# Kernel optimization log

Hardware: AMD Instinct MI355X
Metric: run time of the kernel (lower is better)

## Reference

```python
import jax, jax.numpy as jnp
import numpy as np

N = 100000
BN_EPS = 1e-5


def gcn_conv(x, W, b, src, dst, dinv):
    # PyG GCNConv: out = D^-1/2 (A+I) D^-1/2 (X W) + b
    h = x @ W                                   # [N, out]
    norm = dinv[src] * dinv[dst]                # [E'] edge weights
    msg = h[src] * norm[:, None]                # gather + scale  [E', out]
    agg = jax.ops.segment_sum(msg, dst, num_segments=N)
    return agg + b


def batch_norm(h, gamma, beta):
    mu = jnp.mean(h, axis=0)
    var = jnp.mean((h - mu) ** 2, axis=0)       # biased var, as torch BN training
    return gamma * (h - mu) * jax.lax.rsqrt(var + BN_EPS) + beta


def setup_inputs() -> dict:
    key = jax.random.key(0)
    ks = jax.random.split(key, 12)
    E = 1600000
    d_in, d_h, d_out = 128, 128, 40
    x = jax.random.normal(ks[0], (N, d_in), dtype=jnp.float32)
    edge_index = jax.random.randint(ks[1], (2, E), 0, N, dtype=jnp.int64)

    def glorot(k, fan_in, fan_out):
        s = jnp.sqrt(6.0 / (fan_in + fan_out))
        return jax.random.uniform(k, (fan_in, fan_out), jnp.float32, -s, s)

    return {
        "x": x,
        "W1": glorot(ks[2], d_in, d_h), "b1": jnp.zeros((d_h,), jnp.float32),
        "W2": glorot(ks[3], d_h, d_h), "b2": jnp.zeros((d_h,), jnp.float32),
        "W3": glorot(ks[4], d_h, d_out), "b3": jnp.zeros((d_out,), jnp.float32),
        "g1": 1.0 + 0.1 * jax.random.normal(ks[5], (d_h,), jnp.float32),
        "be1": 0.1 * jax.random.normal(ks[6], (d_h,), jnp.float32),
        "g2": 1.0 + 0.1 * jax.random.normal(ks[7], (d_h,), jnp.float32),
        "be2": 0.1 * jax.random.normal(ks[8], (d_h,), jnp.float32),
        "edge_index": edge_index,
    }


def reference(x, W1, b1, W2, b2, W3, b3, g1, be1, g2, be2, edge_index):
    # add self loops once (PyG add_self_loops=True)
    loop = jnp.arange(N, dtype=edge_index.dtype)
    src = jnp.concatenate([edge_index[0], loop])
    dst = jnp.concatenate([edge_index[1], loop])
    deg = jax.ops.segment_sum(jnp.ones_like(src, dtype=x.dtype), dst, num_segments=N)
    dinv = jax.lax.rsqrt(deg)                   # deg >= 1 due to self loops

    h = gcn_conv(x, W1, b1, src, dst, dinv)
    h = jax.nn.relu(batch_norm(h, g1, be1))     # dropout: identity at eval
    h = gcn_conv(h, W2, b2, src, dst, dinv)
    h = jax.nn.relu(batch_norm(h, g2, be2))
    h = gcn_conv(h, W3, b3, src, dst, dinv)
    return jax.nn.log_softmax(h, axis=1)
```

## Files before the change

kernel.cpp:

```cpp
#include <hip/hip_runtime.h>
#include <cstdint>
#include <cstddef>


typedef unsigned int uint32;
typedef __attribute__((ext_vector_type(8))) short bf16x8;
typedef __attribute__((ext_vector_type(4))) float f32x4;

__device__ inline float bl(uint32 u) { uint32 v = u << 16; return __builtin_bit_cast(float, v); }
__device__ inline float bh(uint32 u) { uint32 v = u & 0xffff0000u; return __builtin_bit_cast(float, v); }
__device__ inline uint32 f2b(float f) {
    uint32 u = __builtin_bit_cast(uint32, f);
    return (u + 0x7fffu + ((u >> 16) & 1u)) >> 16;
}
__device__ inline uint32 pack2(float x, float y) { return f2b(x) | (f2b(y) << 16); }

#define MFMA16(a, b, c) __builtin_amdgcn_mfma_f32_16x16x32_bf16(a, b, c, 0, 0, 0)
#define CSR_CH 4096
#define NSTAT 1024


__global__ __launch_bounds__(256) void bucket_hist(const int* __restrict__ dst,
                                                   int* __restrict__ bcntp,
                                                   int E, int NB) {
    __shared__ int lh[1024];
    for (int t = threadIdx.x; t < NB; t += 256) lh[t] = 0;
    __syncthreads();
    int stride = gridDim.x * 256;
    for (int e = blockIdx.x * 256 + threadIdx.x; e < E; e += stride)
        atomicAdd(&lh[dst[e] >> 7], 1);
    __syncthreads();
    for (int t = threadIdx.x; t < NB; t += 256)
        if (lh[t]) atomicAdd(&bcntp[t * 16], lh[t]);
}

__global__ __launch_bounds__(1024) void bucket_scan(const int* __restrict__ bcntp,
                                                    int* __restrict__ boffs,
                                                    int* __restrict__ bcurp, int nb) {
    __shared__ int s[1024];
    int tx = threadIdx.x;
    int v = (tx < nb) ? bcntp[tx * 16] : 0;
    s[tx] = v;
    __syncthreads();
    for (int off = 1; off < 1024; off <<= 1) {
        int t = (tx >= off) ? s[tx - off] : 0;
        __syncthreads();
        s[tx] += t;
        __syncthreads();
    }
    if (tx < nb) {
        int ex = s[tx] - v;
        boffs[tx] = ex;
        bcurp[tx * 16] = ex;
    }
    if (tx == 0) boffs[nb] = s[1023];
}

__global__ __launch_bounds__(256) void bucket_fill2(const int* __restrict__ src,
                                                    const int* __restrict__ dst,
                                                    int* __restrict__ bcurp,
                                                    uint32* __restrict__ bkt,
                                                    int E, int NB) {
    __shared__ int lh[1024];
    __shared__ int lcur[1024];
    int e0 = blockIdx.x * CSR_CH;
    int e1 = e0 + CSR_CH;
    if (e1 > E) e1 = E;
    for (int t = threadIdx.x; t < NB; t += 256) lh[t] = 0;
    __syncthreads();
    for (int e = e0 + threadIdx.x; e < e1; e += 256)
        atomicAdd(&lh[dst[e] >> 7], 1);
    __syncthreads();
    for (int t = threadIdx.x; t < NB; t += 256)
        lcur[t] = lh[t] ? atomicAdd(&bcurp[t * 16], lh[t]) : 0;
    __syncthreads();
    for (int e = e0 + threadIdx.x; e < e1; e += 256) {
        int d = dst[e];
        int b = d >> 7;
        int pos = atomicAdd(&lcur[b], 1);
        bkt[pos] = (uint32)src[e] | ((uint32)(d & 127) << 17);
    }
}

__global__ __launch_bounds__(256) void bucket_csr(const uint32* __restrict__ bkt,
                                                  const int* __restrict__ boffs,
                                                  float* __restrict__ dinv,
                                                  int* __restrict__ offs,
                                                  int* __restrict__ csr, int n) {
    __shared__ int lcnt[128];
    __shared__ int lscan[128];
    __shared__ int lcur[128];
    int b = blockIdx.x;
    int tx = threadIdx.x;
    if (tx < 128) lcnt[tx] = 0;
    __syncthreads();
    int j0 = boffs[b], j1 = boffs[b + 1];
    for (int j = j0 + tx; j < j1; j += 256)
        atomicAdd(&lcnt[bkt[j] >> 17], 1);
    __syncthreads();
    if (tx < 128) lscan[tx] = lcnt[tx];
    __syncthreads();
    for (int off = 1; off < 128; off <<= 1) {
        int v = 0;
        if (tx < 128 && tx >= off) v = lscan[tx - off];
        __syncthreads();
        if (tx < 128) lscan[tx] += v;
        __syncthreads();
    }
    if (tx < 128) {
        int node = b * 128 + tx;
        if (node < n) {
            int o = j0 + lscan[tx] - lcnt[tx];
            offs[node] = o;
            lcur[tx] = o;
            dinv[node] = rsqrtf((float)(lcnt[tx] + 1));
        }
    }
    if (b == gridDim.x - 1 && tx == 0) offs[n] = j1;
    __syncthreads();
    for (int j = j0 + tx; j < j1; j += 256) {
        uint32 e = bkt[j];
        int dloc = e >> 17;
        int pos = atomicAdd(&lcur[dloc], 1);
        csr[pos] = (int)(e & 0x1FFFFu);
    }
}

__global__ __launch_bounds__(256) void wconv(const float* __restrict__ W1,
                                             const float* __restrict__ W2,
                                             const float* __restrict__ W3,
                                             unsigned short* __restrict__ wt1,
                                             unsigned short* __restrict__ wt2,
                                             unsigned short* __restrict__ wt3) {
    int b = blockIdx.x, tx = threadIdx.x;
    if (b < 2) {
        const float* S = b ? W2 : W1;
        unsigned short* D = b ? wt2 : wt1;
        for (int i = tx; i < 128 * 128; i += 256) {
            int k = i >> 7, nn = i & 127;
            D[nn * 128 + k] = (unsigned short)f2b(S[i]);
        }
    } else {
        for (int i = tx; i < 48 * 128; i += 256) {
            int k = i / 48, nn = i - k * 48;
            float v = (nn < 40) ? W3[k * 40 + nn] : 0.f;
            wt3[nn * 128 + k] = (unsigned short)f2b(v);
        }
    }
}


template <bool ABF16, bool BN>
__global__ __launch_bounds__(256) void gemm128m(const void* __restrict__ Av,
                                                const unsigned short* __restrict__ WT,
                                                uint32* __restrict__ C,
                                                const float* __restrict__ dinv, int n,
                                                const float* __restrict__ scale,
                                                const float* __restrict__ shift) {
    __shared__ unsigned short Wls[128 * 128];
    __shared__ unsigned short Als[128 * 128];
    int tx = threadIdx.x;
    int row0 = blockIdx.x * 128;
    {
        const uint4* srcW = (const uint4*)WT;
#pragma unroll
        for (int i = 0; i < 8; i++) {
            int cid = tx + 256 * i;
            int nr = cid >> 4, kb = cid & 15;
            uint4 u = srcW[cid];
            *(uint4*)&Wls[nr * 128 + ((kb ^ (nr & 7)) << 3)] = u;
        }
    }
    int kb = tx & 15;
    if (ABF16) {
        const uint4* src = (const uint4*)Av;
        float4 sA, sB, hA_, hB_;
        if (BN) {
            sA = ((const float4*)scale)[kb * 2];
            sB = ((const float4*)scale)[kb * 2 + 1];
            hA_ = ((const float4*)shift)[kb * 2];
            hB_ = ((const float4*)shift)[kb * 2 + 1];
        }
#pragma unroll
        for (int i = 0; i < 8; i++) {
            int r = (tx >> 4) + 16 * i;
            int gr = row0 + r;
            if (gr >= n) gr = n - 1;
            uint4 u = src[(size_t)gr * 16 + kb];
            if (BN) {
                uint4 o;
                o.x = pack2(fmaxf(0.f, bl(u.x) * sA.x + hA_.x), fmaxf(0.f, bh(u.x) * sA.y + hA_.y));
                o.y = pack2(fmaxf(0.f, bl(u.y) * sA.z + hA_.z), fmaxf(0.f, bh(u.y) * sA.w + hA_.w));
                o.z = pack2(fmaxf(0.f, bl(u.z) * sB.x + hB_.x), fmaxf(0.f, bh(u.z) * sB.y + hB_.y));
                o.w = pack2(fmaxf(0.f, bl(u.w) * sB.z + hB_.z), fmaxf(0.f, bh(u.w) * sB.w + hB_.w));
                u = o;
            }
            *(uint4*)&Als[r * 128 + ((kb ^ (r & 7)) << 3)] = u;
        }
    } else {
        const float4* src = (const float4*)Av;
#pragma unroll
        for (int i = 0; i < 8; i++) {
            int r = (tx >> 4) + 16 * i;
            int gr = row0 + r;
            if (gr >= n) gr = n - 1;
            float4 a = src[(size_t)gr * 32 + kb * 2];
            float4 b = src[(size_t)gr * 32 + kb * 2 + 1];
            uint4 u;
            u.x = pack2(a.x, a.y);
            u.y = pack2(a.z, a.w);
            u.z = pack2(b.x, b.y);
            u.w = pack2(b.z, b.w);
            *(uint4*)&Als[r * 128 + ((kb ^ (r & 7)) << 3)] = u;
        }
    }
    __syncthreads();

    int w = tx >> 6, lane = tx & 63;
    int r0 = w * 32;
    int lrow = lane & 15, lkg = lane >> 4;
    f32x4 acc[2][8];
#pragma unroll
    for (int rt = 0; rt < 2; rt++)
#pragma unroll
        for (int nt = 0; nt < 8; nt++) acc[rt][nt] = (f32x4){0.f, 0.f, 0.f, 0.f};
#pragma unroll
    for (int ks = 0; ks < 4; ks++) {
        int kbl = ks * 4 + lkg;
        int r = r0 + lrow;
        bf16x8 a0 = *(const bf16x8*)&Als[r * 128 + ((kbl ^ (r & 7)) << 3)];
        int r2 = r0 + 16 + lrow;
        bf16x8 a1 = *(const bf16x8*)&Als[r2 * 128 + ((kbl ^ (r2 & 7)) << 3)];
#pragma unroll
        for (int nt = 0; nt < 8; nt++) {
            int nr = nt * 16 + lrow;
            bf16x8 b = *(const bf16x8*)&Wls[nr * 128 + ((kbl ^ (nr & 7)) << 3)];
            acc[0][nt] = MFMA16(a0, b, acc[0][nt]);
            acc[1][nt] = MFMA16(a1, b, acc[1][nt]);
        }
    }
    float* SL = (float*)&Als[w * 4096];
#pragma unroll
    for (int rt = 0; rt < 2; rt++) {
#pragma unroll
        for (int nt = 0; nt < 8; nt++)
#pragma unroll
            for (int j = 0; j < 4; j++)
                SL[(lkg * 4 + j) * 128 + nt * 16 + lrow] = acc[rt][nt][j];
#pragma unroll
        for (int i = 0; i < 8; i++) {
            int rloc = i * 2 + (lane >> 5);
            int gr = row0 + r0 + rt * 16 + rloc;
            int cq = lane & 31;
            if (gr < n) {
                float dv = dinv[gr];
                float4 v = *(float4*)&SL[rloc * 128 + cq * 4];
                uint2 o;
                o.x = pack2(v.x * dv, v.y * dv);
                o.y = pack2(v.z * dv, v.w * dv);
                *(uint2*)&C[(size_t)gr * 64 + cq * 2] = o;
            }
        }
        if (rt == 0) __builtin_amdgcn_s_waitcnt(0);
    }
}

__global__ __launch_bounds__(256) void gemm40m(const uint32* __restrict__ A,
                                               const unsigned short* __restrict__ WT,
                                               unsigned short* __restrict__ C,
                                               const float* __restrict__ dinv, int n,
                                               const float* __restrict__ scale,
                                               const float* __restrict__ shift) {
    __shared__ unsigned short Wls[48 * 128];
    __shared__ unsigned short Als[128 * 128];
    int tx = threadIdx.x;
    int row0 = blockIdx.x * 128;
    {
        const uint4* srcW = (const uint4*)WT;
#pragma unroll
        for (int i = 0; i < 3; i++) {
            int cid = tx + 256 * i;
            int nr = cid >> 4, kb = cid & 15;
            uint4 u = srcW[cid];
            *(uint4*)&Wls[nr * 128 + ((kb ^ (nr & 7)) << 3)] = u;
        }
    }
    int kb = tx & 15;
    {
        const uint4* src = (const uint4*)A;
        float4 sA = ((const float4*)scale)[kb * 2];
        float4 sB = ((const float4*)scale)[kb * 2 + 1];
        float4 hA_ = ((const float4*)shift)[kb * 2];
        float4 hB_ = ((const float4*)shift)[kb * 2 + 1];
#pragma unroll
        for (int i = 0; i < 8; i++) {
            int r = (tx >> 4) + 16 * i;
            int gr = row0 + r;
            if (gr >= n) gr = n - 1;
            uint4 u = src[(size_t)gr * 16 + kb];
            uint4 o;
            o.x = pack2(fmaxf(0.f, bl(u.x) * sA.x + hA_.x), fmaxf(0.f, bh(u.x) * sA.y + hA_.y));
            o.y = pack2(fmaxf(0.f, bl(u.y) * sA.z + hA_.z), fmaxf(0.f, bh(u.y) * sA.w + hA_.w));
            o.z = pack2(fmaxf(0.f, bl(u.z) * sB.x + hB_.x), fmaxf(0.f, bh(u.z) * sB.y + hB_.y));
            o.w = pack2(fmaxf(0.f, bl(u.w) * sB.z + hB_.z), fmaxf(0.f, bh(u.w) * sB.w + hB_.w));
            *(uint4*)&Als[r * 128 + ((kb ^ (r & 7)) << 3)] = o;
        }
    }
    __syncthreads();

    int w = tx >> 6, lane = tx & 63;
    int r0 = w * 32;
    int lrow = lane & 15, lkg = lane >> 4;
    f32x4 acc[2][3];
#pragma unroll
    for (int rt = 0; rt < 2; rt++)
#pragma unroll
        for (int nt = 0; nt < 3; nt++) acc[rt][nt] = (f32x4){0.f, 0.f, 0.f, 0.f};
#pragma unroll
    for (int ks = 0; ks < 4; ks++) {
        int kbl = ks * 4 + lkg;
        int r = r0 + lrow;
        bf16x8 a0 = *(const bf16x8*)&Als[r * 128 + ((kbl ^ (r & 7)) << 3)];
        int r2 = r0 + 16 + lrow;
        bf16x8 a1 = *(const bf16x8*)&Als[r2 * 128 + ((kbl ^ (r2 & 7)) << 3)];
#pragma unroll
        for (int nt = 0; nt < 3; nt++) {
            int nr = nt * 16 + lrow;
            bf16x8 b = *(const bf16x8*)&Wls[nr * 128 + ((kbl ^ (nr & 7)) << 3)];
            acc[0][nt] = MFMA16(a0, b, acc[0][nt]);
            acc[1][nt] = MFMA16(a1, b, acc[1][nt]);
        }
    }
#pragma unroll
    for (int rt = 0; rt < 2; rt++)
#pragma unroll
        for (int j = 0; j < 4; j++) {
            int gr = row0 + r0 + rt * 16 + lkg * 4 + j;
            if (gr < n) {
                float dv = dinv[gr];
#pragma unroll
                for (int nt = 0; nt < 3; nt++) {
                    int col = nt * 16 + lrow;
                    if (col < 40)
                        C[(size_t)gr * 40 + col] = (unsigned short)f2b(acc[rt][nt][j] * dv);
                }
            }
        }
}


__global__ __launch_bounds__(256) void agg128(const uint32* __restrict__ h,
                                              const int* __restrict__ csr,
                                              const int* __restrict__ offs,
                                              const float* __restrict__ dinv,
                                              const float* __restrict__ bias,
                                              uint32* __restrict__ out, int n) {
    int wid = (blockIdx.x * 256 + threadIdx.x) >> 6;
    int lane = threadIdx.x & 63;
    if (wid >= n) return;
    int half = lane >> 5;
    int t = lane & 31;
    const uint2* h2 = (const uint2*)h;
    float a0 = 0.f, a1 = 0.f, a2 = 0.f, a3 = 0.f;
    float c0 = 0.f, c1 = 0.f, c2 = 0.f, c3 = 0.f;
    if (half == 0) {
        uint2 u = h2[(size_t)wid * 32 + t];
        a0 = bl(u.x); a1 = bh(u.x); a2 = bl(u.y); a3 = bh(u.y);
    }
    int e0 = offs[wid], e1 = offs[wid + 1];
    int e = e0;
    while (e < e1) {
        int cnt = e1 - e;
        if (cnt > 64) cnt = 64;
        int sl = (lane < cnt) ? csr[e + lane] : 0;
        int j = 0;
        for (; j + 3 < cnt; j += 4) {
            int sa = __shfl(sl, j + half, 64);
            int sb = __shfl(sl, j + 2 + half, 64);
            uint2 ua = h2[(size_t)sa * 32 + t];
            uint2 ub = h2[(size_t)sb * 32 + t];
            a0 += bl(ua.x); a1 += bh(ua.x); a2 += bl(ua.y); a3 += bh(ua.y);
            c0 += bl(ub.x); c1 += bh(ub.x); c2 += bl(ub.y); c3 += bh(ub.y);
        }
        for (; j < cnt; j++) {
            int s = __shfl(sl, j, 64);
            if (half == (j & 1)) {
                uint2 u = h2[(size_t)s * 32 + t];
                a0 += bl(u.x); a1 += bh(u.x); a2 += bl(u.y); a3 += bh(u.y);
            }
        }
        e += cnt;
    }
    a0 += c0; a1 += c1; a2 += c2; a3 += c3;
    a0 += __shfl_xor(a0, 32, 64);
    a1 += __shfl_xor(a1, 32, 64);
    a2 += __shfl_xor(a2, 32, 64);
    a3 += __shfl_xor(a3, 32, 64);
    if (half == 0) {
        float di = dinv[wid];
        float4 bb = ((const float4*)bias)[t];
        uint2 o;
        o.x = pack2(a0 * di + bb.x, a1 * di + bb.y);
        o.y = pack2(a2 * di + bb.z, a3 * di + bb.w);
        ((uint2*)out)[(size_t)wid * 32 + t] = o;
    }
}

__global__ __launch_bounds__(256) void agg40_lsm(const uint32* __restrict__ h,
                                                 const int* __restrict__ csr,
                                                 const int* __restrict__ offs,
                                                 const float* __restrict__ dinv,
                                                 const float* __restrict__ bias,
                                                 float* __restrict__ out, int n) {
    int wid = (blockIdx.x * 256 + threadIdx.x) >> 6;
    int lane = threadIdx.x & 63;
    if (wid >= n) return;
    int grp = lane / 10;
    int t = lane - grp * 10;
    bool work = grp < 6;
    const uint2* h2 = (const uint2*)h;
    float a0 = 0.f, a1 = 0.f, a2 = 0.f, a3 = 0.f;
    if (grp == 0) {
        uint2 u = h2[(size_t)wid * 10 + t];
        a0 = bl(u.x); a1 = bh(u.x); a2 = bl(u.y); a3 = bh(u.y);
    }
    int e0 = offs[wid], e1 = offs[wid + 1];
    int e = e0;
    while (e < e1) {
        int cnt = e1 - e;
        if (cnt > 64) cnt = 64;
        int sl = (lane < cnt) ? csr[e + lane] : 0;
        int nIt = (cnt + 11) / 12;
        for (int it = 0; it < nIt; it++) {
            int j0 = it * 12 + grp;
            int j1 = j0 + 6;
            int s0 = __shfl(sl, (j0 < cnt) ? j0 : 0, 64);
            int s1 = __shfl(sl, (j1 < cnt) ? j1 : 0, 64);
            if (work && j0 < cnt) {
                uint2 u = h2[(size_t)s0 * 10 + t];
                a0 += bl(u.x); a1 += bh(u.x); a2 += bl(u.y); a3 += bh(u.y);
            }
            if (work && j1 < cnt) {
                uint2 u = h2[(size_t)s1 * 10 + t];
                a0 += bl(u.x); a1 += bh(u.x); a2 += bl(u.y); a3 += bh(u.y);
            }
        }
        e += cnt;
    }
    a0 += __shfl(a0, (lane + 30) & 63, 64);
    a1 += __shfl(a1, (lane + 30) & 63, 64);
    a2 += __shfl(a2, (lane + 30) & 63, 64);
    a3 += __shfl(a3, (lane + 30) & 63, 64);
    {
        float t0 = __shfl(a0, (lane + 10) & 63, 64), u0 = __shfl(a0, (lane + 20) & 63, 64);
        float t1 = __shfl(a1, (lane + 10) & 63, 64), u1 = __shfl(a1, (lane + 20) & 63, 64);
        float t2 = __shfl(a2, (lane + 10) & 63, 64), u2 = __shfl(a2, (lane + 20) & 63, 64);
        float t3 = __shfl(a3, (lane + 10) & 63, 64), u3 = __shfl(a3, (lane + 20) & 63, 64);
        a0 += t0 + u0; a1 += t1 + u1; a2 += t2 + u2; a3 += t3 + u3;
    }
    bool act = lane < 10;
    float di = dinv[wid];
    float v0 = -1e30f, v1 = -1e30f, v2 = -1e30f, v3 = -1e30f;
    if (act) {
        float4 bb = ((const float4*)bias)[t];
        v0 = a0 * di + bb.x;
        v1 = a1 * di + bb.y;
        v2 = a2 * di + bb.z;
        v3 = a3 * di + bb.w;
    }
    float m = fmaxf(fmaxf(v0, v1), fmaxf(v2, v3));
    for (int off = 8; off; off >>= 1) m = fmaxf(m, __shfl_xor(m, off, 64));
    float ss = act ? (expf(v0 - m) + expf(v1 - m) + expf(v2 - m) + expf(v3 - m)) : 0.f;
    for (int off = 8; off; off >>= 1) ss += __shfl_xor(ss, off, 64);
    float lg = logf(ss);
    if (act) {
        float4 o = {v0 - m - lg, v1 - m - lg, v2 - m - lg, v3 - m - lg};
        *(float4*)&out[(size_t)wid * 40 + t * 4] = o;
    }
}


__global__ __launch_bounds__(256) void stats_k(const uint32* __restrict__ h,
                                               float* __restrict__ psum,
                                               float* __restrict__ psq, int n) {
    int kb = threadIdx.x & 15;
    int rg = threadIdx.x >> 4;
    float s[8], q[8];
#pragma unroll
    for (int j = 0; j < 8; j++) { s[j] = 0.f; q[j] = 0.f; }
    const uint4* h4 = (const uint4*)h;
    for (int r = blockIdx.x * 16 + rg; r < n; r += gridDim.x * 16) {
        uint4 u = h4[(size_t)r * 16 + kb];
        float f[8] = {bl(u.x), bh(u.x), bl(u.y), bh(u.y),
                      bl(u.z), bh(u.z), bl(u.w), bh(u.w)};
#pragma unroll
        for (int j = 0; j < 8; j++) { s[j] += f[j]; q[j] += f[j] * f[j]; }
    }
    __shared__ float LS[16][16][8];
    __shared__ float LQ[16][16][8];
#pragma unroll
    for (int j = 0; j < 8; j++) { LS[rg][kb][j] = s[j]; LQ[rg][kb][j] = q[j]; }
    __syncthreads();
    if (threadIdx.x < 128) {
        int cq = threadIdx.x >> 3, j = threadIdx.x & 7;
        float S = 0.f, Q = 0.f;
#pragma unroll
        for (int g = 0; g < 16; g++) { S += LS[g][cq][j]; Q += LQ[g][cq][j]; }
        psum[blockIdx.x * 128 + cq * 8 + j] = S;
        psq[blockIdx.x * 128 + cq * 8 + j] = Q;
    }
}

__global__ __launch_bounds__(1024) void finalize_stats(const float* __restrict__ psum,
                                                       const float* __restrict__ psq,
                                                       const float* __restrict__ g,
                                                       const float* __restrict__ be,
                                                       float* __restrict__ scale,
                                                       float* __restrict__ shift,
                                                       int nb, float invN) {
    int c = threadIdx.x & 127;
    int seg = threadIdx.x >> 7;
    int per = nb >> 3;
    float s = 0.f, q = 0.f;
    for (int b = seg * per; b < (seg + 1) * per; b++) {
        s += psum[b * 128 + c];
        q += psq[b * 128 + c];
    }
    __shared__ float LS[8][128], LQ[8][128];
    LS[seg][c] = s;
    LQ[seg][c] = q;
    __syncthreads();
    if (threadIdx.x < 128) {
        float S = 0.f, Q = 0.f;
#pragma unroll
        for (int g2 = 0; g2 < 8; g2++) { S += LS[g2][c]; Q += LQ[g2][c]; }
        float mu = S * invN;
        float var = Q * invN - mu * mu;
        float sc = g[c] * rsqrtf(var + 1e-5f);
        scale[c] = sc;
        shift[c] = be[c] - mu * sc;
    }
}

extern "C" void kernel_launch(void* const* d_in, const int* in_sizes, int n_in,
                              void* d_out, int out_size, void* d_ws, size_t ws_size,
                              hipStream_t stream) {
    const float* x   = (const float*)d_in[0];
    const float* W1  = (const float*)d_in[1];
    const float* b1  = (const float*)d_in[2];
    const float* W2  = (const float*)d_in[3];
    const float* b2  = (const float*)d_in[4];
    const float* W3  = (const float*)d_in[5];
    const float* b3  = (const float*)d_in[6];
    const float* g1  = (const float*)d_in[7];
    const float* be1 = (const float*)d_in[8];
    const float* g2  = (const float*)d_in[9];
    const float* be2 = (const float*)d_in[10];
    const int*   ei  = (const int*)d_in[11];

    int n = in_sizes[0] / 128;
    int E = in_sizes[11] / 2;
    const int* src = ei;
    const int* dst = ei + E;
    int NB = (n + 127) >> 7;

    char* p = (char*)d_ws;
    size_t off = 0;
    auto alloc = [&](size_t bytes) -> void* {
        off = (off + 255) & ~(size_t)255;
        void* r = p + off;
        off += bytes;
        return r;
    };
    uint32* hA    = (uint32*)alloc((size_t)n * 64 * 4);
    uint32* hB    = (uint32*)alloc((size_t)n * 64 * 4);
    float* dinv   = (float*)alloc((size_t)n * 4);
    int*   offs   = (int*)alloc((size_t)(n + 1) * 4);
    int*   csr    = (int*)alloc((size_t)E * 4);
    float* psum   = (float*)alloc((size_t)NSTAT * 128 * 4);
    float* psq    = (float*)alloc((size_t)NSTAT * 128 * 4);
    float* scale  = (float*)alloc(128 * 4);
    float* shift  = (float*)alloc(128 * 4);
    unsigned short* wt1 = (unsigned short*)alloc(128 * 128 * 2);
    unsigned short* wt2 = (unsigned short*)alloc(128 * 128 * 2);
    unsigned short* wt3 = (unsigned short*)alloc(48 * 128 * 2);
    int*   bcntp  = (int*)alloc((size_t)NB * 16 * 4);
    int*   boffs  = (int*)alloc((size_t)(NB + 1) * 4);
    int*   bcurp  = (int*)alloc((size_t)NB * 16 * 4);
    uint32* bkt   = hA;
    (void)ws_size;

    int gG = (n + 127) / 128;
    int gAgg = (n * 64 + 255) / 256;
    int gFill = (E + CSR_CH - 1) / CSR_CH;
    float invN = 1.0f / (float)n;

    hipMemsetAsync(bcntp, 0, (size_t)NB * 16 * 4, stream);

    wconv<<<3, 256, 0, stream>>>(W1, W2, W3, wt1, wt2, wt3);
    bucket_hist<<<256, 256, 0, stream>>>(dst, bcntp, E, NB);
    bucket_scan<<<1, 1024, 0, stream>>>(bcntp, boffs, bcurp, NB);
    bucket_fill2<<<gFill, 256, 0, stream>>>(src, dst, bcurp, bkt, E, NB);
    bucket_csr<<<NB, 256, 0, stream>>>(bkt, boffs, dinv, offs, csr, n);

    gemm128m<false, false><<<gG, 256, 0, stream>>>(x, wt1, hA, dinv, n, nullptr, nullptr);
    agg128<<<gAgg, 256, 0, stream>>>(hA, csr, offs, dinv, b1, hB, n);
    stats_k<<<NSTAT, 256, 0, stream>>>(hB, psum, psq, n);
    finalize_stats<<<1, 1024, 0, stream>>>(psum, psq, g1, be1, scale, shift, NSTAT, invN);

    gemm128m<true, true><<<gG, 256, 0, stream>>>(hB, wt2, hA, dinv, n, scale, shift);
    agg128<<<gAgg, 256, 0, stream>>>(hA, csr, offs, dinv, b2, hB, n);
    stats_k<<<NSTAT, 256, 0, stream>>>(hB, psum, psq, n);
    finalize_stats<<<1, 1024, 0, stream>>>(psum, psq, g2, be2, scale, shift, NSTAT, invN);

    gemm40m<<<gG, 256, 0, stream>>>(hB, wt3, (unsigned short*)hA, dinv, n, scale, shift);
    agg40_lsm<<<gAgg, 256, 0, stream>>>(hA, csr, offs, dinv, b3, (float*)d_out, n);
}
```

Baseline: 429.5 us.

## Fuse batch-norm statistics accumulation into the aggregation kernel

The aggregation kernel becomes a persistent grid-stride kernel with a fixed grid, and each block accumulates per-column sums and sums of squares of its output rows. It then writes block partials for finalize_stats, so the separate stats pass that re-read the aggregated tensor is removed. In exchange, the grid for the gather-heavy kernel is fixed at 2048 blocks, which may reduce latency hiding or load balance. Statistics are now computed on fp32 values before bf16 rounding, which differs slightly from the old path.

Result: slower. 495.3 us (+15.3%).

```diff
diff --git a/kernel.cpp b/kernel.cpp
--- a/kernel.cpp
+++ b/kernel.cpp
@@ -17,7 +17,7 @@
 
 #define MFMA16(a, b, c) __builtin_amdgcn_mfma_f32_16x16x32_bf16(a, b, c, 0, 0, 0)
 #define CSR_CH 4096
-#define NSTAT 1024
+#define GSTAT 2048
 
 
 __global__ __launch_bounds__(256) void bucket_hist(const int* __restrict__ dst,
@@ -349,60 +349,87 @@
 }
 
 
-__global__ __launch_bounds__(256) void agg128(const uint32* __restrict__ h,
-                                              const int* __restrict__ csr,
-                                              const int* __restrict__ offs,
-                                              const float* __restrict__ dinv,
-                                              const float* __restrict__ bias,
-                                              uint32* __restrict__ out, int n) {
-    int wid = (blockIdx.x * 256 + threadIdx.x) >> 6;
+__global__ __launch_bounds__(256) void agg128s(const uint32* __restrict__ h,
+                                               const int* __restrict__ csr,
+                                               const int* __restrict__ offs,
+                                               const float* __restrict__ dinv,
+                                               const float* __restrict__ bias,
+                                               uint32* __restrict__ out,
+                                               float* __restrict__ psum,
+                                               float* __restrict__ psq, int n) {
+    int w = threadIdx.x >> 6;
     int lane = threadIdx.x & 63;
-    if (wid >= n) return;
     int half = lane >> 5;
     int t = lane & 31;
     const uint2* h2 = (const uint2*)h;
-    float a0 = 0.f, a1 = 0.f, a2 = 0.f, a3 = 0.f;
-    float c0 = 0.f, c1 = 0.f, c2 = 0.f, c3 = 0.f;
+    float4 bb = ((const float4*)bias)[t];
+    float s0 = 0.f, s1 = 0.f, s2 = 0.f, s3 = 0.f;
+    float q0 = 0.f, q1 = 0.f, q2 = 0.f, q3 = 0.f;
+    for (int wid = blockIdx.x * 4 + w; wid < n; wid += gridDim.x * 4) {
+        float a0 = 0.f, a1 = 0.f, a2 = 0.f, a3 = 0.f;
+        float c0 = 0.f, c1 = 0.f, c2 = 0.f, c3 = 0.f;
+        if (half == 0) {
+            uint2 u = h2[(size_t)wid * 32 + t];
+            a0 = bl(u.x); a1 = bh(u.x); a2 = bl(u.y); a3 = bh(u.y);
+        }
+        int e0 = offs[wid], e1 = offs[wid + 1];
+        int e = e0;
+        while (e < e1) {
+            int cnt = e1 - e;
+            if (cnt > 64) cnt = 64;
+            int sl = (lane < cnt) ? csr[e + lane] : 0;
+            int j = 0;
+            for (; j + 3 < cnt; j += 4) {
+                int sa = __shfl(sl, j + half, 64);
+                int sb = __shfl(sl, j + 2 + half, 64);
+                uint2 ua = h2[(size_t)sa * 32 + t];
+                uint2 ub = h2[(size_t)sb * 32 + t];
+                a0 += bl(ua.x); a1 += bh(ua.x); a2 += bl(ua.y); a3 += bh(ua.y);
+                c0 += bl(ub.x); c1 += bh(ub.x); c2 += bl(ub.y); c3 += bh(ub.y);
+            }
+            for (; j < cnt; j++) {
+                int s = __shfl(sl, j, 64);
+                if (half == (j & 1)) {
+                    uint2 u = h2[(size_t)s * 32 + t];
+                    a0 += bl(u.x); a1 += bh(u.x); a2 += bl(u.y); a3 += bh(u.y);
+                }
+            }
+            e += cnt;
+        }
+        a0 += c0; a1 += c1; a2 += c2; a3 += c3;
+        a0 += __shfl_xor(a0, 32, 64);
+        a1 += __shfl_xor(a1, 32, 64);
+        a2 += __shfl_xor(a2, 32, 64);
+        a3 += __shfl_xor(a3, 32, 64);
+        if (half == 0) {
+            float di = dinv[wid];
+            float v0 = a0 * di + bb.x;
+            float v1 = a1 * di + bb.y;
+            float v2 = a2 * di + bb.z;
+            float v3 = a3 * di + bb.w;
+            s0 += v0; q0 += v0 * v0;
+            s1 += v1; q1 += v1 * v1;
+            s2 += v2; q2 += v2 * v2;
+            s3 += v3; q3 += v3 * v3;
+            uint2 o;
+            o.x = pack2(v0, v1);
+            o.y = pack2(v2, v3);
+            ((uint2*)out)[(size_t)wid * 32 + t] = o;
+        }
+    }
+    __shared__ float LS[4][32][4], LQ[4][32][4];
     if (half == 0) {
-        uint2 u = h2[(size_t)wid * 32 + t];
-        a0 = bl(u.x); a1 = bh(u.x); a2 = bl(u.y); a3 = bh(u.y);
-    }
-    int e0 = offs[wid], e1 = offs[wid + 1];
-    int e = e0;
-    while (e < e1) {
-        int cnt = e1 - e;
-        if (cnt > 64) cnt = 64;
-        int sl = (lane < cnt) ? csr[e + lane] : 0;
-        int j = 0;
-        for (; j + 3 < cnt; j += 4) {
-            int sa = __shfl(sl, j + half, 64);
-            int sb = __shfl(sl, j + 2 + half, 64);
-            uint2 ua = h2[(size_t)sa * 32 + t];
-            uint2 ub = h2[(size_t)sb * 32 + t];
-            a0 += bl(ua.x); a1 += bh(ua.x); a2 += bl(ua.y); a3 += bh(ua.y);
-            c0 += bl(ub.x); c1 += bh(ub.x); c2 += bl(ub.y); c3 += bh(ub.y);
-        }
-        for (; j < cnt; j++) {
-            int s = __shfl(sl, j, 64);
-            if (half == (j & 1)) {
-                uint2 u = h2[(size_t)s * 32 + t];
-                a0 += bl(u.x); a1 += bh(u.x); a2 += bl(u.y); a3 += bh(u.y);
-            }
-        }
-        e += cnt;
-    }
-    a0 += c0; a1 += c1; a2 += c2; a3 += c3;
-    a0 += __shfl_xor(a0, 32, 64);
-    a1 += __shfl_xor(a1, 32, 64);
-    a2 += __shfl_xor(a2, 32, 64);
-    a3 += __shfl_xor(a3, 32, 64);
-    if (half == 0) {
-        float di = dinv[wid];
-        float4 bb = ((const float4*)bias)[t];
-        uint2 o;
-        o.x = pack2(a0 * di + bb.x, a1 * di + bb.y);
-        o.y = pack2(a2 * di + bb.z, a3 * di + bb.w);
-        ((uint2*)out)[(size_t)wid * 32 + t] = o;
+        LS[w][t][0] = s0; LS[w][t][1] = s1; LS[w][t][2] = s2; LS[w][t][3] = s3;
+        LQ[w][t][0] = q0; LQ[w][t][1] = q1; LQ[w][t][2] = q2; LQ[w][t][3] = q3;
+    }
+    __syncthreads();
+    if (threadIdx.x < 128) {
+        int cq = threadIdx.x >> 2, j = threadIdx.x & 3;
+        float S = 0.f, Q = 0.f;
+#pragma unroll
+        for (int g = 0; g < 4; g++) { S += LS[g][cq][j]; Q += LQ[g][cq][j]; }
+        psum[blockIdx.x * 128 + threadIdx.x] = S;
+        psq[blockIdx.x * 128 + threadIdx.x] = Q;
     }
 }
 
@@ -480,37 +507,6 @@
 }
 
 
-__global__ __launch_bounds__(256) void stats_k(const uint32* __restrict__ h,
-                                               float* __restrict__ psum,
-                                               float* __restrict__ psq, int n) {
-    int kb = threadIdx.x & 15;
-    int rg = threadIdx.x >> 4;
-    float s[8], q[8];
-#pragma unroll
-    for (int j = 0; j < 8; j++) { s[j] = 0.f; q[j] = 0.f; }
-    const uint4* h4 = (const uint4*)h;
-    for (int r = blockIdx.x * 16 + rg; r < n; r += gridDim.x * 16) {
-        uint4 u = h4[(size_t)r * 16 + kb];
-        float f[8] = {bl(u.x), bh(u.x), bl(u.y), bh(u.y),
-                      bl(u.z), bh(u.z), bl(u.w), bh(u.w)};
-#pragma unroll
-        for (int j = 0; j < 8; j++) { s[j] += f[j]; q[j] += f[j] * f[j]; }
-    }
-    __shared__ float LS[16][16][8];
-    __shared__ float LQ[16][16][8];
-#pragma unroll
-    for (int j = 0; j < 8; j++) { LS[rg][kb][j] = s[j]; LQ[rg][kb][j] = q[j]; }
-    __syncthreads();
-    if (threadIdx.x < 128) {
-        int cq = threadIdx.x >> 3, j = threadIdx.x & 7;
-        float S = 0.f, Q = 0.f;
-#pragma unroll
-        for (int g = 0; g < 16; g++) { S += LS[g][cq][j]; Q += LQ[g][cq][j]; }
-        psum[blockIdx.x * 128 + cq * 8 + j] = S;
-        psq[blockIdx.x * 128 + cq * 8 + j] = Q;
-    }
-}
-
 __global__ __launch_bounds__(1024) void finalize_stats(const float* __restrict__ psum,
                                                        const float* __restrict__ psq,
                                                        const float* __restrict__ g,
@@ -577,8 +573,8 @@
     float* dinv   = (float*)alloc((size_t)n * 4);
     int*   offs   = (int*)alloc((size_t)(n + 1) * 4);
     int*   csr    = (int*)alloc((size_t)E * 4);
-    float* psum   = (float*)alloc((size_t)NSTAT * 128 * 4);
-    float* psq    = (float*)alloc((size_t)NSTAT * 128 * 4);
+    float* psum   = (float*)alloc((size_t)GSTAT * 128 * 4);
+    float* psq    = (float*)alloc((size_t)GSTAT * 128 * 4);
     float* scale  = (float*)alloc(128 * 4);
     float* shift  = (float*)alloc(128 * 4);
     unsigned short* wt1 = (unsigned short*)alloc(128 * 128 * 2);
@@ -604,14 +600,12 @@
     bucket_csr<<<NB, 256, 0, stream>>>(bkt, boffs, dinv, offs, csr, n);
 
     gemm128m<false, false><<<gG, 256, 0, stream>>>(x, wt1, hA, dinv, n, nullptr, nullptr);
-    agg128<<<gAgg, 256, 0, stream>>>(hA, csr, offs, dinv, b1, hB, n);
-    stats_k<<<NSTAT, 256, 0, stream>>>(hB, psum, psq, n);
-    finalize_stats<<<1, 1024, 0, stream>>>(psum, psq, g1, be1, scale, shift, NSTAT, invN);
+    agg128s<<<GSTAT, 256, 0, stream>>>(hA, csr, offs, dinv, b1, hB, psum, psq, n);
+    finalize_stats<<<1, 1024, 0, stream>>>(psum, psq, g1, be1, scale, shift, GSTAT, invN);
 
     gemm128m<true, true><<<gG, 256, 0, stream>>>(hB, wt2, hA, dinv, n, scale, shift);
-    agg128<<<gAgg, 256, 0, stream>>>(hA, csr, offs, dinv, b2, hB, n);
-    stats_k<<<NSTAT, 256, 0, stream>>>(hB, psum, psq, n);
-    finalize_stats<<<1, 1024, 0, stream>>>(psum, psq, g2, be2, scale, shift, NSTAT, invN);
+    agg128s<<<GSTAT, 256, 0, stream>>>(hA, csr, offs, dinv, b2, hB, psum, psq, n);
+    finalize_stats<<<1, 1024, 0, stream>>>(psum, psq, g2, be2, scale, shift, GSTAT, invN);
 
     gemm40m<<<gG, 256, 0, stream>>>(hB, wt3, (unsigned short*)hA, dinv, n, scale, shift);
     agg40_lsm<<<gAgg, 256, 0, stream>>>(hA, csr, offs, dinv, b3, (float*)d_out, n);
```
